# Kernel tuning notes

Measured on AMD Instinct MI355X. Metric: run time of the kernel, lower is better.

Reference implementation:

```python
import jax, jax.numpy as jnp
import numpy as np

B, S, D = 2, 1024, 2048
H, HK, HD = 16, 4, 128
E, TOPK, I = 16, 6, 1024
IS = 2048  # shared experts intermediate = moe_intermediate_size[0] * moe_num_shared_experts
EPS = 1e-6
NORM_MIN = 1e-12
SCALE = HD ** -0.5


def setup_inputs() -> dict:
    key = jax.random.key(0)
    ks = jax.random.split(key, 16)
    w = lambda k, *sh: jax.random.normal(k, sh, jnp.float32) * 0.02
    # interleaved RoPE tables (rotate_half_text pairs even/odd dims)
    inv_freq = 1.0 / (10000.0 ** (np.arange(0, HD, 2, dtype=np.float32) / HD))
    freqs = np.outer(np.arange(S, dtype=np.float32), inv_freq)        # [S, HD/2]
    emb = np.repeat(freqs, 2, axis=-1)                                 # [S, HD]
    cos = jnp.asarray(np.broadcast_to(np.cos(emb)[None], (B, S, HD)).copy())
    sin = jnp.asarray(np.broadcast_to(np.sin(emb)[None], (B, S, HD)).copy())
    return dict(
        hidden_states=jax.random.normal(ks[0], (B, S, D), jnp.float32),
        cos=cos, sin=sin,
        ln1_w=jnp.ones((D,), jnp.float32),
        ln2_w=jnp.ones((D,), jnp.float32),
        Wq=w(ks[1], D, H * HD), Wk=w(ks[2], D, HK * HD), Wv=w(ks[3], D, HK * HD), Wo=w(ks[4], H * HD, D),
        Wgate=w(ks[5], D, E),
        corr_bias=jnp.zeros((E,), jnp.float32),
        Wg=w(ks[6], E, D, I), Wu=w(ks[7], E, D, I), Wd=w(ks[8], E, I, D),
        Wgs=w(ks[9], D, IS), Wus=w(ks[10], D, IS), Wds=w(ks[11], IS, D),
    )


def rms_norm(x, weight, eps=EPS):
    xf = x.astype(jnp.float32)
    var = jnp.mean(xf * xf, axis=-1, keepdims=True)
    return (weight * (xf * jax.lax.rsqrt(var + eps))).astype(x.dtype)


def rotate_half(x):
    # interleaved variant: (x0, x1, x2, x3, ...) -> (-x1, x0, -x3, x2, ...)
    x1 = x[..., 0::2]
    x2 = x[..., 1::2]
    return jnp.stack((-x2, x1), axis=-1).reshape(x.shape)


def apply_rope(q, k, cos, sin):
    # q: [B,H,S,HD], k: [B,HK,S,HD], cos/sin: [B,S,HD] -> unsqueeze head dim
    c = cos[:, None].astype(jnp.float32)
    s = sin[:, None].astype(jnp.float32)
    qe = (q.astype(jnp.float32) * c + rotate_half(q).astype(jnp.float32) * s).astype(q.dtype)
    ke = (k.astype(jnp.float32) * c + rotate_half(k).astype(jnp.float32) * s).astype(k.dtype)
    return qe, ke


def attention(x, cos, sin, Wq, Wk, Wv, Wo):
    b, s, _ = x.shape
    q = (x @ Wq).reshape(b, s, H, HD).transpose(0, 2, 1, 3)    # [B,H,S,HD]
    k = (x @ Wk).reshape(b, s, HK, HD).transpose(0, 2, 1, 3)   # [B,HK,S,HD]
    v = (x @ Wv).reshape(b, s, HK, HD).transpose(0, 2, 1, 3)
    q, k = apply_rope(q, k, cos, sin)
    rep = H // HK
    k = jnp.repeat(k, rep, axis=1)
    v = jnp.repeat(v, rep, axis=1)
    scores = jnp.einsum('bhqd,bhkd->bhqk', q, k).astype(jnp.float32) * SCALE
    mask = jnp.triu(jnp.full((s, s), jnp.finfo(jnp.float32).min, jnp.float32), 1)
    attn = jax.nn.softmax(scores + mask, axis=-1).astype(x.dtype)
    out = jnp.einsum('bhqk,bhkd->bhqd', attn, v)
    out = out.transpose(0, 2, 1, 3).reshape(b, s, H * HD)
    return out @ Wo


def moe(x, Wgate, corr_bias, Wg, Wu, Wd, Wgs, Wus, Wds):
    b, s, d = x.shape
    # shared experts (dense SwiGLU MLP)
    shared = (jax.nn.silu(x @ Wgs) * (x @ Wus)) @ Wds
    xt = x.reshape(-1, d)                                       # [T, D]
    T = xt.shape[0]
    logits = xt.astype(jnp.float32) @ Wgate                     # float32 gate
    probs = jax.nn.softmax(logits, axis=-1)
    _, sel = jax.lax.top_k(probs + corr_bias, TOPK)             # [T, K]
    rw = jnp.take_along_axis(probs, sel, axis=-1)               # gather un-corrected probs
    rw = rw / jnp.clip(jnp.sum(rw, axis=-1, keepdims=True), NORM_MIN)
    # dense routing matrix [T, E] (zero for unselected experts == index_add semantics)
    route = jnp.zeros((T, E), jnp.float32).at[jnp.arange(T)[:, None], sel].set(rw)
    route = route.astype(x.dtype)
    # run all experts densely, mask with routing weights
    g = jnp.einsum('td,edi->tei', xt, Wg)
    u = jnp.einsum('td,edi->tei', xt, Wu)
    eo = jnp.einsum('tei,eid->ted', jax.nn.silu(g) * u, Wd)     # per-expert down proj
    y = jnp.einsum('ted,te->td', eo, route).reshape(b, s, d)
    return y + shared


def reference(hidden_states, cos, sin, ln1_w, ln2_w, Wq, Wk, Wv, Wo,
              Wgate, corr_bias, Wg, Wu, Wd, Wgs, Wus, Wds):
    residual = hidden_states
    h = rms_norm(hidden_states, ln1_w)
    h = attention(h, cos, sin, Wq, Wk, Wv, Wo)
    h = residual + h
    residual = h
    h = rms_norm(h, ln2_w)
    h = moe(h, Wgate, corr_bias, Wg, Wu, Wd, Wgs, Wus, Wds)
    return residual + h
```

## Files before the change

kernel.cpp:

```cpp
#include <hip/hip_runtime.h>
#include <cstdint>

typedef unsigned short u16;
typedef __attribute__((ext_vector_type(8))) short short8;
typedef __attribute__((ext_vector_type(4))) short s16x4;
typedef __attribute__((ext_vector_type(4))) float f32x4;

#define MFMA_16x16x32(a,b,c) __builtin_amdgcn_mfma_f32_16x16x32_bf16(a,b,c,0,0,0)

#define GLDS16(lds, g) __builtin_amdgcn_global_load_lds( \
    (const __attribute__((address_space(1))) unsigned int*)(g), \
    (__attribute__((address_space(3))) unsigned int*)(lds), 16, 0, 0)

#define BB 2
#define SS 1024
#define DD 2048
#define HH 16
#define HKK 4
#define HDD 128
#define EE 16
#define NTOP 6
#define II 1024
#define ISS 2048
#define TT 2048
#define CAP 2048

__device__ __forceinline__ u16 f2b(float f) {
    union { float f; uint32_t u; } v; v.f = f;
    uint32_t r = v.u + 0x7FFFu + ((v.u >> 16) & 1u);
    return (u16)(r >> 16);
}
__device__ __forceinline__ float b2f(u16 h) {
    union { uint32_t u; float f; } v; v.u = ((uint32_t)h) << 16;
    return v.f;
}
__device__ __forceinline__ void fsplit(float f, u16& hi, u16& lo) {
    u16 h = f2b(f);
    hi = h;
    lo = f2b(f - b2f(h));
}

template<bool SPLIT>
__global__ __launch_bounds__(256) void k_prep(
    const float* __restrict__ In, u16* __restrict__ Oh, u16* __restrict__ Ol,
    int R, int C)
{
    const size_t zoff = (size_t)blockIdx.z * R * C;
    In += zoff; Oh += zoff; if (SPLIT) Ol += zoff;
    const int r0 = blockIdx.y * 32, c0 = blockIdx.x * 32;
    __shared__ float tile[32][33];
    const int tx = threadIdx.x & 31, ty = threadIdx.x >> 5;
    #pragma unroll
    for (int i = 0; i < 4; ++i)
        tile[ty + i*8][tx] = In[(size_t)(r0 + ty + i*8)*C + c0 + tx];
    __syncthreads();
    const int c = threadIdx.x >> 3, rs = (threadIdx.x & 7) * 4;
    s16x4 hv, lv;
    #pragma unroll
    for (int j = 0; j < 4; ++j) {
        float f = tile[rs + j][c];
        u16 hb = f2b(f);
        hv[j] = (short)hb;
        if (SPLIT) lv[j] = (short)f2b(f - b2f(hb));
        else lv[j] = 0;
    }
    *(s16x4*)(Oh + (size_t)(c0 + c)*R + r0 + rs) = hv;
    if (SPLIT) *(s16x4*)(Ol + (size_t)(c0 + c)*R + r0 + rs) = lv;
}

__global__ __launch_bounds__(256) void k_rmsnorm_split(
    const float* __restrict__ X, const float* __restrict__ Wt,
    u16* __restrict__ Oh, u16* __restrict__ Ol)
{
    const int t = blockIdx.x;
    const float* x = X + (size_t)t * DD;
    const int base = threadIdx.x * 8;
    f32x4 v0 = *(const f32x4*)(x + base);
    f32x4 v1 = *(const f32x4*)(x + base + 4);
    float ss = 0.f;
    #pragma unroll
    for (int j = 0; j < 4; ++j) ss += v0[j]*v0[j] + v1[j]*v1[j];
    #pragma unroll
    for (int o = 1; o < 64; o <<= 1) ss += __shfl_xor(ss, o);
    __shared__ float red[4];
    if ((threadIdx.x & 63) == 0) red[threadIdx.x >> 6] = ss;
    __syncthreads();
    float tot = red[0] + red[1] + red[2] + red[3];
    float inv = rsqrtf(tot * (1.0f/DD) + 1e-6f);
    f32x4 w0 = *(const f32x4*)(Wt + base);
    f32x4 w1 = *(const f32x4*)(Wt + base + 4);
    u16* oh = Oh + (size_t)t*DD + base;
    u16* ol = Ol + (size_t)t*DD + base;
    #pragma unroll
    for (int j = 0; j < 4; ++j) {
        float y0 = v0[j]*inv*w0[j];
        float y1 = v1[j]*inv*w1[j];
        fsplit(y0, oh[j],   ol[j]);
        fsplit(y1, oh[4+j], ol[4+j]);
    }
}

__global__ __launch_bounds__(256) void k_rmsnorm_bf(
    const float* __restrict__ X, const float* __restrict__ Wt,
    u16* __restrict__ Ob, float* __restrict__ Of)
{
    const int t = blockIdx.x;
    const float* x = X + (size_t)t * DD;
    const int base = threadIdx.x * 8;
    f32x4 v0 = *(const f32x4*)(x + base);
    f32x4 v1 = *(const f32x4*)(x + base + 4);
    float ss = 0.f;
    #pragma unroll
    for (int j = 0; j < 4; ++j) ss += v0[j]*v0[j] + v1[j]*v1[j];
    #pragma unroll
    for (int o = 1; o < 64; o <<= 1) ss += __shfl_xor(ss, o);
    __shared__ float red[4];
    if ((threadIdx.x & 63) == 0) red[threadIdx.x >> 6] = ss;
    __syncthreads();
    float tot = red[0] + red[1] + red[2] + red[3];
    float inv = rsqrtf(tot * (1.0f/DD) + 1e-6f);
    f32x4 w0 = *(const f32x4*)(Wt + base);
    f32x4 w1 = *(const f32x4*)(Wt + base + 4);
    u16* ob = Ob + (size_t)t*DD + base;
    float* of = Of + (size_t)t*DD + base;
    #pragma unroll
    for (int j = 0; j < 4; ++j) {
        float y0 = v0[j]*inv*w0[j];
        float y1 = v1[j]*inv*w1[j];
        ob[j] = f2b(y0); ob[4+j] = f2b(y1);
        of[j] = y0;      of[4+j] = y1;
    }
}

template<int EPI>
__global__ __launch_bounds__(256) void k_gemm_hi(
    const u16* __restrict__ Ah, const u16* __restrict__ Al,
    const u16* __restrict__ Bth, const u16* __restrict__ Btl,
    float* __restrict__ C, const float* __restrict__ Res,
    int M, int N, int K)
{
    __shared__ u16 Ash[128][32];
    __shared__ u16 Asl[128][32];
    __shared__ u16 Bsh[128][32];
    __shared__ u16 Bsl[128][32];
    const int tid = threadIdx.x;
    const int lane = tid & 63;
    const int w = tid >> 6;
    const int m0 = blockIdx.y * 128, n0 = blockIdx.x * 128;
    const int wm = (w >> 1) * 64, wn = (w & 1) * 64;
    const int l15 = lane & 15, lhi = lane >> 4;
    f32x4 acc[4][4];
    #pragma unroll
    for (int a = 0; a < 4; ++a)
        #pragma unroll
        for (int b = 0; b < 4; ++b) acc[a][b] = 0;

    const int gr = w*32 + (lane >> 2);
    const int gc = (lane & 3) * 8;
    const u16* ahP0 = Ah  + (size_t)(m0 + gr) * K + gc;
    const u16* alP0 = Al  + (size_t)(m0 + gr) * K + gc;
    const u16* bhP0 = Bth + (size_t)(n0 + gr) * K + gc;
    const u16* blP0 = Btl + (size_t)(n0 + gr) * K + gc;
    const size_t r16 = (size_t)16 * K;

    for (int k0 = 0; k0 < K; k0 += 32) {
        __syncthreads();
        GLDS16(&Ash[w*32][0],      ahP0 + k0);
        GLDS16(&Ash[w*32 + 16][0], ahP0 + r16 + k0);
        GLDS16(&Asl[w*32][0],      alP0 + k0);
        GLDS16(&Asl[w*32 + 16][0], alP0 + r16 + k0);
        GLDS16(&Bsh[w*32][0],      bhP0 + k0);
        GLDS16(&Bsh[w*32 + 16][0], bhP0 + r16 + k0);
        GLDS16(&Bsl[w*32][0],      blP0 + k0);
        GLDS16(&Bsl[w*32 + 16][0], blP0 + r16 + k0);
        __syncthreads();
        short8 afh[4], afl[4], bfh[4], bfl[4];
        #pragma unroll
        for (int i = 0; i < 4; ++i) {
            afh[i] = *(const short8*)&Ash[wm + i*16 + l15][lhi*8];
            afl[i] = *(const short8*)&Asl[wm + i*16 + l15][lhi*8];
            bfh[i] = *(const short8*)&Bsh[wn + i*16 + l15][lhi*8];
            bfl[i] = *(const short8*)&Bsl[wn + i*16 + l15][lhi*8];
        }
        #pragma unroll
        for (int a = 0; a < 4; ++a)
            #pragma unroll
            for (int b = 0; b < 4; ++b) {
                acc[a][b] = MFMA_16x16x32(afh[a], bfh[b], acc[a][b]);
                acc[a][b] = MFMA_16x16x32(afh[a], bfl[b], acc[a][b]);
                acc[a][b] = MFMA_16x16x32(afl[a], bfh[b], acc[a][b]);
            }
    }
    #pragma unroll
    for (int a = 0; a < 4; ++a)
      #pragma unroll
      for (int b = 0; b < 4; ++b)
        #pragma unroll
        for (int r = 0; r < 4; ++r) {
            int m = m0 + wm + a*16 + lhi*4 + r;
            int n = n0 + wn + b*16 + l15;
            size_t off = (size_t)m * N + n;
            float v = acc[a][b][r];
            if (EPI == 1) C[off] = v + Res[off];
            else C[off] = v;
        }
}

template<int EPI>
__global__ __launch_bounds__(256) void k_gemm(
    const u16* __restrict__ A, const u16* __restrict__ Bt,
    void* __restrict__ C, int M, int N, int K)
{
    __shared__ u16 As[128][32];
    __shared__ u16 Bs[128][32];
    const int tid = threadIdx.x;
    const int lane = tid & 63;
    const int w = tid >> 6;
    const int m0 = blockIdx.y * 128, n0 = blockIdx.x * 128;
    const int wm = (w >> 1) * 64, wn = (w & 1) * 64;
    const int l15 = lane & 15, lhi = lane >> 4;
    f32x4 acc[4][4];
    #pragma unroll
    for (int a = 0; a < 4; ++a)
        #pragma unroll
        for (int b = 0; b < 4; ++b) acc[a][b] = 0;

    const int gr = w*32 + (lane >> 2);
    const int gc = (lane & 3) * 8;
    const u16* aP0 = A  + (size_t)(m0 + gr) * K + gc;
    const u16* bP0 = Bt + (size_t)(n0 + gr) * K + gc;
    const size_t r16 = (size_t)16 * K;

    for (int k0 = 0; k0 < K; k0 += 32) {
        __syncthreads();
        GLDS16(&As[w*32][0],      aP0 + k0);
        GLDS16(&As[w*32 + 16][0], aP0 + r16 + k0);
        GLDS16(&Bs[w*32][0],      bP0 + k0);
        GLDS16(&Bs[w*32 + 16][0], bP0 + r16 + k0);
        __syncthreads();
        short8 af[4], bf[4];
        #pragma unroll
        for (int i = 0; i < 4; ++i) af[i] = *(const short8*)&As[wm + i*16 + l15][lhi*8];
        #pragma unroll
        for (int i = 0; i < 4; ++i) bf[i] = *(const short8*)&Bs[wn + i*16 + l15][lhi*8];
        #pragma unroll
        for (int a = 0; a < 4; ++a)
            #pragma unroll
            for (int b = 0; b < 4; ++b)
                acc[a][b] = MFMA_16x16x32(af[a], bf[b], acc[a][b]);
    }
    #pragma unroll
    for (int a = 0; a < 4; ++a)
      #pragma unroll
      for (int b = 0; b < 4; ++b)
        #pragma unroll
        for (int r = 0; r < 4; ++r) {
            int m = m0 + wm + a*16 + lhi*4 + r;
            int n = n0 + wn + b*16 + l15;
            size_t off = (size_t)m * N + n;
            float v = acc[a][b][r];
            if (EPI == 0) ((u16*)C)[off] = f2b(v);
            else ((float*)C)[off] = v;
        }
}

template<bool GATHER>
__global__ __launch_bounds__(256) void k_glu(
    const u16* __restrict__ Xb, const u16* __restrict__ W1t,
    const u16* __restrict__ W2t, u16* __restrict__ Hout,
    const int* __restrict__ list, const int* __restrict__ cntp,
    int M, int NE, int K)
{
    const int e = GATHER ? blockIdx.z : 0;
    const int cnt = GATHER ? cntp[e] : M;
    const int m0 = blockIdx.y * 128;
    if (m0 >= cnt) return;
    const int n0 = blockIdx.x * 64;
    const u16* w1 = W1t + (size_t)e * NE * K;
    const u16* w2 = W2t + (size_t)e * NE * K;
    u16* hout = Hout + (size_t)e * CAP * NE;
    const int* lst = GATHER ? (list + e * CAP) : nullptr;

    __shared__ u16 As[128][32];
    __shared__ u16 B1s[64][32];
    __shared__ u16 B2s[64][32];

    const int tid = threadIdx.x, lane = tid & 63, w = tid >> 6;
    const int wm = (w >> 1) * 64, wn = (w & 1) * 32;
    const int l15 = lane & 15, lhi = lane >> 4;
    f32x4 acc1[4][2], acc2[4][2];
    #pragma unroll
    for (int a = 0; a < 4; ++a)
        #pragma unroll
        for (int j = 0; j < 2; ++j) { acc1[a][j] = 0; acc2[a][j] = 0; }

    const int gr  = w*32 + (lane >> 2);
    const int grB = w*16 + (lane >> 2);
    const int gc  = (lane & 3) * 8;
    int arow0, arow1;
    if (GATHER) {
        int mr0 = m0 + gr, mr1 = m0 + gr + 16;
        arow0 = (mr0 < cnt) ? (lst[mr0] >> 3) : 0;
        arow1 = (mr1 < cnt) ? (lst[mr1] >> 3) : 0;
    } else { arow0 = m0 + gr; arow1 = m0 + gr + 16; }
    const u16* aP0 = Xb + (size_t)arow0 * K + gc;
    const u16* aP1 = Xb + (size_t)arow1 * K + gc;
    const u16* b1P = w1 + (size_t)(n0 + grB) * K + gc;
    const u16* b2P = w2 + (size_t)(n0 + grB) * K + gc;

    for (int k0 = 0; k0 < K; k0 += 32) {
        __syncthreads();
        GLDS16(&As[w*32][0],      aP0 + k0);
        GLDS16(&As[w*32 + 16][0], aP1 + k0);
        GLDS16(&B1s[w*16][0],     b1P + k0);
        GLDS16(&B2s[w*16][0],     b2P + k0);
        __syncthreads();
        short8 af[4], b1[2], b2[2];
        #pragma unroll
        for (int i = 0; i < 4; ++i) af[i] = *(const short8*)&As[wm + i*16 + l15][lhi*8];
        #pragma unroll
        for (int j = 0; j < 2; ++j) {
            b1[j] = *(const short8*)&B1s[wn + j*16 + l15][lhi*8];
            b2[j] = *(const short8*)&B2s[wn + j*16 + l15][lhi*8];
        }
        #pragma unroll
        for (int a = 0; a < 4; ++a)
            #pragma unroll
            for (int j = 0; j < 2; ++j) {
                acc1[a][j] = MFMA_16x16x32(af[a], b1[j], acc1[a][j]);
                acc2[a][j] = MFMA_16x16x32(af[a], b2[j], acc2[a][j]);
            }
    }
    #pragma unroll
    for (int a = 0; a < 4; ++a)
      #pragma unroll
      for (int j = 0; j < 2; ++j)
        #pragma unroll
        for (int r = 0; r < 4; ++r) {
            int m = m0 + wm + a*16 + lhi*4 + r;
            if (m < cnt) {
                int n = n0 + wn + j*16 + l15;
                float g = acc1[a][j][r], u = acc2[a][j][r];
                float hval = g / (1.0f + __expf(-g)) * u;
                hout[(size_t)m * NE + n] = f2b(hval);
            }
        }
}

__global__ __launch_bounds__(256) void k_down_scatter(
    const u16* __restrict__ Hb, const u16* __restrict__ WdTt,
    u16* __restrict__ Rbuf, const int* __restrict__ list,
    const float* __restrict__ wts, const int* __restrict__ cntp,
    int N, int K)
{
    const int e = blockIdx.z;
    const int cnt = cntp[e];
    const int m0 = blockIdx.y * 128;
    if (m0 >= cnt) return;
    const int n0 = blockIdx.x * 128;
    const u16* A  = Hb   + (size_t)e * CAP * K;
    const u16* Bt = WdTt + (size_t)e * N * K;

    __shared__ u16 As[128][32];
    __shared__ u16 Bs[128][32];
    const int tid = threadIdx.x, lane = tid & 63, w = tid >> 6;
    const int wm = (w >> 1) * 64, wn = (w & 1) * 64;
    const int l15 = lane & 15, lhi = lane >> 4;
    f32x4 acc[4][4];
    #pragma unroll
    for (int a = 0; a < 4; ++a)
        #pragma unroll
        for (int b = 0; b < 4; ++b) acc[a][b] = 0;

    const int gr = w*32 + (lane >> 2);
    const int gc = (lane & 3) * 8;
    const u16* aP0 = A  + (size_t)(m0 + gr) * K + gc;
    const u16* bP0 = Bt + (size_t)(n0 + gr) * K + gc;
    const size_t r16 = (size_t)16 * K;

    for (int k0 = 0; k0 < K; k0 += 32) {
        __syncthreads();
        GLDS16(&As[w*32][0],      aP0 + k0);
        GLDS16(&As[w*32 + 16][0], aP0 + r16 + k0);
        GLDS16(&Bs[w*32][0],      bP0 + k0);
        GLDS16(&Bs[w*32 + 16][0], bP0 + r16 + k0);
        __syncthreads();
        short8 af[4], bf[4];
        #pragma unroll
        for (int i = 0; i < 4; ++i) af[i] = *(const short8*)&As[wm + i*16 + l15][lhi*8];
        #pragma unroll
        for (int i = 0; i < 4; ++i) bf[i] = *(const short8*)&Bs[wn + i*16 + l15][lhi*8];
        #pragma unroll
        for (int a = 0; a < 4; ++a)
            #pragma unroll
            for (int b = 0; b < 4; ++b)
                acc[a][b] = MFMA_16x16x32(af[a], bf[b], acc[a][b]);
    }
    #pragma unroll
    for (int a = 0; a < 4; ++a)
      #pragma unroll
      for (int b = 0; b < 4; ++b)
        #pragma unroll
        for (int r = 0; r < 4; ++r) {
            int m = m0 + wm + a*16 + lhi*4 + r;
            if (m < cnt) {
                int n = n0 + wn + b*16 + l15;
                int enc = list[e*CAP + m];
                float wgt = wts[e*CAP + m];
                int tok = enc >> 3, kk = enc & 7;
                Rbuf[((size_t)tok*NTOP + kk)*N + n] = f2b(acc[a][b][r] * wgt);
            }
        }
}

__global__ __launch_bounds__(256) void k_rope_f32(
    float* __restrict__ QKV,
    const float* __restrict__ Cs, const float* __restrict__ Sn)
{
    int id = blockIdx.x * 256 + threadIdx.x;
    int pr = id & 63;
    int rest = id >> 6;
    int hh = rest % 20;
    int tok = rest / 20;
    if (tok >= TT) return;
    int d0 = pr * 2;
    float c0 = Cs[(size_t)tok*HDD + d0];
    float c1 = Cs[(size_t)tok*HDD + d0 + 1];
    float s0 = Sn[(size_t)tok*HDD + d0];
    float s1 = Sn[(size_t)tok*HDD + d0 + 1];
    float* p = QKV + (size_t)tok*3072 + (hh < HH ? hh*HDD : 2048 + (hh - HH)*HDD);
    float x0 = p[d0], x1 = p[d0+1];
    p[d0]     = x0*c0 - x1*s0;
    p[d0 + 1] = x1*c1 + x0*s1;
}

__global__ __launch_bounds__(256) void k_split_s(
    const float* __restrict__ X, int stride, int cols,
    u16* __restrict__ Hi, u16* __restrict__ Lo)
{
    int id = blockIdx.x * 256 + threadIdx.x;
    int base = id * 8;
    int t = base / cols;
    int c = base - t * cols;
    const float* in = X + (size_t)t * stride + c;
    f32x4 v0 = *(const f32x4*)in;
    f32x4 v1 = *(const f32x4*)(in + 4);
    u16* h = Hi + (size_t)t * cols + c;
    u16* l = Lo + (size_t)t * cols + c;
    #pragma unroll
    for (int j = 0; j < 4; ++j) {
        fsplit(v0[j], h[j],   l[j]);
        fsplit(v1[j], h[4+j], l[4+j]);
    }
}

__global__ __launch_bounds__(256) void k_split_vt(
    const float* __restrict__ QKV, u16* __restrict__ Vth, u16* __restrict__ Vtl)
{
    int id = blockIdx.x * 256 + threadIdx.x;
    int oid = id * 8;
    int s0 = oid & (SS - 1);
    int r = oid >> 10;
    int d = r & (HDD - 1);
    int bh = r >> 7;
    int b = bh >> 2, hk = bh & 3;
    #pragma unroll
    for (int j = 0; j < 8; ++j) {
        int s = s0 + j;
        float v = QKV[(size_t)(b*SS + s)*3072 + 2560 + hk*HDD + d];
        fsplit(v, Vth[oid + j], Vtl[oid + j]);
    }
}

__global__ __launch_bounds__(256) void k_attn_hi(
    const u16* __restrict__ Qh, const u16* __restrict__ Ql,
    const u16* __restrict__ Kh, const u16* __restrict__ Kl,
    const u16* __restrict__ Vth, const u16* __restrict__ Vtl,
    u16* __restrict__ Oh, u16* __restrict__ Ol)
{
    const int tid = threadIdx.x;
    const int lane = tid & 63;
    const int w = tid >> 6;
    const int q0 = blockIdx.x * 64;
    const int b = blockIdx.y >> 4;
    const int h = blockIdx.y & 15;
    const int hk = h >> 2;
    const int l15 = lane & 15, lhi = lane >> 4;

    __shared__ u16 Ksh[32][136];
    __shared__ u16 Ksl[32][136];
    __shared__ u16 Vsh[128][40];
    __shared__ u16 Vsl[128][40];
    __shared__ u16 Psh[4][16][40];
    __shared__ u16 Psl[4][16][40];

    short8 qfh[4], qfl[4];
    {
        const int qrow = q0 + w*16 + l15;
        const u16* qph = Qh + ((size_t)(b*SS + qrow)*HH + h)*HDD;
        const u16* qpl = Ql + ((size_t)(b*SS + qrow)*HH + h)*HDD;
        #pragma unroll
        for (int c = 0; c < 4; ++c) {
            qfh[c] = *(const short8*)(qph + c*32 + lhi*8);
            qfl[c] = *(const short8*)(qpl + c*32 + lhi*8);
        }
    }

    f32x4 oacc[8];
    #pragma unroll
    for (int ch = 0; ch < 8; ++ch) oacc[ch] = 0;
    float m_r[4] = {-1e30f, -1e30f, -1e30f, -1e30f};
    float l_r[4] = {0.f, 0.f, 0.f, 0.f};

    const int nkt = (q0 + 64) >> 5;
    const int kr = tid >> 3, kc = (tid & 7) * 16;
    const int vd = tid >> 1, vj = (tid & 1) * 16;

    for (int kt = 0; kt < nkt; ++kt) {
        __syncthreads();
        {
            size_t koff = ((size_t)(b*SS + kt*32 + kr)*HKK + hk)*HDD + kc;
            *(short8*)&Ksh[kr][kc]     = *(const short8*)(Kh + koff);
            *(short8*)&Ksh[kr][kc + 8] = *(const short8*)(Kh + koff + 8);
            *(short8*)&Ksl[kr][kc]     = *(const short8*)(Kl + koff);
            *(short8*)&Ksl[kr][kc + 8] = *(const short8*)(Kl + koff + 8);
        }
        {
            size_t voff = ((size_t)(b*HKK + hk)*HDD + vd)*SS + kt*32 + vj;
            *(short8*)&Vsh[vd][vj]     = *(const short8*)(Vth + voff);
            *(short8*)&Vsh[vd][vj + 8] = *(const short8*)(Vth + voff + 8);
            *(short8*)&Vsl[vd][vj]     = *(const short8*)(Vtl + voff);
            *(short8*)&Vsl[vd][vj + 8] = *(const short8*)(Vtl + voff + 8);
        }
        __syncthreads();

        f32x4 s0 = 0, s1 = 0;
        #pragma unroll
        for (int c = 0; c < 4; ++c) {
            short8 kh0 = *(const short8*)&Ksh[l15][c*32 + lhi*8];
            short8 kl0 = *(const short8*)&Ksl[l15][c*32 + lhi*8];
            short8 kh1 = *(const short8*)&Ksh[16 + l15][c*32 + lhi*8];
            short8 kl1 = *(const short8*)&Ksl[16 + l15][c*32 + lhi*8];
            s0 = MFMA_16x16x32(qfh[c], kh0, s0);
            s0 = MFMA_16x16x32(qfh[c], kl0, s0);
            s0 = MFMA_16x16x32(qfl[c], kh0, s0);
            s1 = MFMA_16x16x32(qfh[c], kh1, s1);
            s1 = MFMA_16x16x32(qfh[c], kl1, s1);
            s1 = MFMA_16x16x32(qfl[c], kh1, s1);
        }
        const int irow0 = q0 + w*16 + lhi*4;
        const int j0 = kt*32 + l15;
        float ef[4];
        #pragma unroll
        for (int r = 0; r < 4; ++r) {
            float a0 = s0[r] * 0.08838834764831845f;
            float a1 = s1[r] * 0.08838834764831845f;
            const int ir = irow0 + r;
            if (j0 > ir) a0 = -1e30f;
            if (j0 + 16 > ir) a1 = -1e30f;
            float mx = fmaxf(a0, a1);
            #pragma unroll
            for (int o = 1; o < 16; o <<= 1) mx = fmaxf(mx, __shfl_xor(mx, o));
            float mn = fmaxf(m_r[r], mx);
            ef[r] = __expf(m_r[r] - mn);
            m_r[r] = mn;
            float p0 = __expf(a0 - mn);
            float p1 = __expf(a1 - mn);
            float ps = p0 + p1;
            #pragma unroll
            for (int o = 1; o < 16; o <<= 1) ps += __shfl_xor(ps, o);
            l_r[r] = l_r[r]*ef[r] + ps;
            fsplit(p0, Psh[w][lhi*4 + r][l15],      Psl[w][lhi*4 + r][l15]);
            fsplit(p1, Psh[w][lhi*4 + r][16 + l15], Psl[w][lhi*4 + r][16 + l15]);
        }
        #pragma unroll
        for (int ch = 0; ch < 8; ++ch) {
            f32x4 t = oacc[ch];
            t[0] *= ef[0]; t[1] *= ef[1]; t[2] *= ef[2]; t[3] *= ef[3];
            oacc[ch] = t;
        }
        __syncthreads();
        short8 pah = *(const short8*)&Psh[w][l15][lhi*8];
        short8 pal = *(const short8*)&Psl[w][l15][lhi*8];
        #pragma unroll
        for (int ch = 0; ch < 8; ++ch) {
            short8 bvh = *(const short8*)&Vsh[ch*16 + l15][lhi*8];
            short8 bvl = *(const short8*)&Vsl[ch*16 + l15][lhi*8];
            oacc[ch] = MFMA_16x16x32(pah, bvh, oacc[ch]);
            oacc[ch] = MFMA_16x16x32(pah, bvl, oacc[ch]);
            oacc[ch] = MFMA_16x16x32(pal, bvh, oacc[ch]);
        }
    }
    #pragma unroll
    for (int r = 0; r < 4; ++r) {
        const int row = q0 + w*16 + lhi*4 + r;
        const float inv = 1.0f / l_r[r];
        u16* oph = Oh + ((size_t)(b*SS + row)*HH + h)*HDD;
        u16* opl = Ol + ((size_t)(b*SS + row)*HH + h)*HDD;
        #pragma unroll
        for (int ch = 0; ch < 8; ++ch) {
            float o = oacc[ch][r] * inv;
            fsplit(o, oph[ch*16 + l15], opl[ch*16 + l15]);
        }
    }
}

__global__ __launch_bounds__(256) void k_router(
    const float* __restrict__ X, const float* __restrict__ Wg,
    const float* __restrict__ bias,
    int* __restrict__ cnt, int* __restrict__ list, float* __restrict__ wts)
{
    const int t = blockIdx.x;
    const int e = threadIdx.x & 15, sl = threadIdx.x >> 4;
    const float* x = X + (size_t)t * DD;
    float part = 0.f;
    for (int i = 0; i < 128; ++i) {
        int k = sl * 128 + i;
        part += x[k] * Wg[(size_t)k * EE + e];
    }
    __shared__ float red[16][17];
    red[sl][e] = part;
    __syncthreads();
    if (threadIdx.x == 0) {
        float lg[16], pr[16];
        for (int ee = 0; ee < 16; ++ee) {
            float s = 0.f;
            for (int q = 0; q < 16; ++q) s += red[q][ee];
            lg[ee] = s;
        }
        float mx = lg[0];
        for (int ee = 1; ee < 16; ++ee) mx = fmaxf(mx, lg[ee]);
        float sum = 0.f;
        for (int ee = 0; ee < 16; ++ee) { pr[ee] = expf(lg[ee] - mx); sum += pr[ee]; }
        float isum = 1.0f / sum;
        for (int ee = 0; ee < 16; ++ee) pr[ee] *= isum;
        unsigned used = 0;
        int sel[NTOP]; float rw[NTOP]; float s6 = 0.f;
        for (int kk = 0; kk < NTOP; ++kk) {
            int best = 0; float bv = -1e30f;
            for (int ee = 0; ee < 16; ++ee) {
                if (used & (1u << ee)) continue;
                float sc = pr[ee] + bias[ee];
                if (sc > bv) { bv = sc; best = ee; }
            }
            used |= 1u << best;
            sel[kk] = best; rw[kk] = pr[best]; s6 += pr[best];
        }
        float inv6 = 1.0f / fmaxf(s6, 1e-12f);
        for (int kk = 0; kk < NTOP; ++kk) {
            int ee = sel[kk];
            int pos = atomicAdd(&cnt[ee], 1);
            list[ee*CAP + pos] = (t << 3) | kk;
            wts[ee*CAP + pos] = rw[kk] * inv6;
        }
    }
}

__global__ __launch_bounds__(256) void k_final(
    const float* __restrict__ h2, const float* __restrict__ yb,
    const u16* __restrict__ rb, float* __restrict__ out)
{
    int id = blockIdx.x * 256 + threadIdx.x;
    size_t i4 = (size_t)id * 4;
    int t = id >> 9;
    int d = (id & 511) * 4;
    f32x4 acc = *(const f32x4*)(h2 + i4);
    f32x4 y = *(const f32x4*)(yb + i4);
    acc += y;
    #pragma unroll
    for (int kk = 0; kk < NTOP; ++kk) {
        s16x4 rv = *(const s16x4*)(rb + ((size_t)t*NTOP + kk)*DD + d);
        acc[0] += b2f((u16)rv[0]); acc[1] += b2f((u16)rv[1]);
        acc[2] += b2f((u16)rv[2]); acc[3] += b2f((u16)rv[3]);
    }
    *(f32x4*)(out + i4) = acc;
}

extern "C" void kernel_launch(void* const* d_in, const int* in_sizes, int n_in,
                              void* d_out, int out_size, void* d_ws, size_t ws_size,
                              hipStream_t stream)
{
    (void)in_sizes; (void)n_in; (void)out_size; (void)ws_size;
    const float* hidden = (const float*)d_in[0];
    const float* cosb   = (const float*)d_in[1];
    const float* sinb   = (const float*)d_in[2];
    const float* ln1    = (const float*)d_in[3];
    const float* ln2    = (const float*)d_in[4];
    const float* Wq     = (const float*)d_in[5];
    const float* Wk     = (const float*)d_in[6];
    const float* Wv     = (const float*)d_in[7];
    const float* Wo     = (const float*)d_in[8];
    const float* Wgate  = (const float*)d_in[9];
    const float* cbias  = (const float*)d_in[10];
    const float* Wg     = (const float*)d_in[11];
    const float* Wu     = (const float*)d_in[12];
    const float* Wd     = (const float*)d_in[13];
    const float* Wgs    = (const float*)d_in[14];
    const float* Wus    = (const float*)d_in[15];
    const float* Wds    = (const float*)d_in[16];
    float* out = (float*)d_out;

    char* ws = (char*)d_ws;
    size_t off = 0;
    auto alloc = [&](size_t bytes) {
        void* p = ws + off;
        off = (off + bytes + 255) & ~(size_t)255;
        return p;
    };
    u16* WqkvTh = (u16*)alloc((size_t)3072*2048*2);
    u16* WqkvTl = (u16*)alloc((size_t)3072*2048*2);
    u16* WoTh   = (u16*)alloc((size_t)2048*2048*2);
    u16* WoTl   = (u16*)alloc((size_t)2048*2048*2);
    u16* WgsT   = (u16*)alloc((size_t)2048*2048*2);
    u16* WusT   = (u16*)alloc((size_t)2048*2048*2);
    u16* WdsT   = (u16*)alloc((size_t)2048*2048*2);
    u16* WgT    = (u16*)alloc((size_t)EE*II*DD*2);
    u16* WuT    = (u16*)alloc((size_t)EE*II*DD*2);
    u16* WdT    = (u16*)alloc((size_t)EE*DD*II*2);
    u16*   x1h  = (u16*)  alloc((size_t)TT*DD*2);
    u16*   x1l  = (u16*)  alloc((size_t)TT*DD*2);
    float* qkvf = (float*)alloc((size_t)TT*3072*4);
    u16*   qh   = (u16*)  alloc((size_t)TT*HH*HDD*2);
    u16*   ql   = (u16*)  alloc((size_t)TT*HH*HDD*2);
    u16*   kh   = (u16*)  alloc((size_t)TT*HKK*HDD*2);
    u16*   kl   = (u16*)  alloc((size_t)TT*HKK*HDD*2);
    u16*   vth  = (u16*)  alloc((size_t)TT*HKK*HDD*2);
    u16*   vtl  = (u16*)  alloc((size_t)TT*HKK*HDD*2);
    u16*   aoh  = (u16*)  alloc((size_t)TT*HH*HDD*2);
    u16*   aol  = (u16*)  alloc((size_t)TT*HH*HDD*2);
    float* h2   = (float*)alloc((size_t)TT*DD*4);
    u16*   x2   = (u16*)  alloc((size_t)TT*DD*2);
    float* x2f  = (float*)alloc((size_t)TT*DD*4);
    int*   cnt  = (int*)  alloc(256);
    int*   lst  = (int*)  alloc((size_t)EE*CAP*4);
    float* wts  = (float*)alloc((size_t)EE*CAP*4);
    u16*   hE   = (u16*)  alloc((size_t)EE*CAP*II*2);
    u16*   rbuf = (u16*)  alloc((size_t)TT*NTOP*DD*2);
    u16*   hs   = x1h;
    float* ybuf = qkvf;

    k_prep<true ><<<dim3(64,64,1), 256, 0, stream>>>(Wq, WqkvTh, WqkvTl, 2048, 2048);
    k_prep<true ><<<dim3(16,64,1), 256, 0, stream>>>(Wk, WqkvTh + (size_t)2048*2048, WqkvTl + (size_t)2048*2048, 2048, 512);
    k_prep<true ><<<dim3(16,64,1), 256, 0, stream>>>(Wv, WqkvTh + (size_t)2560*2048, WqkvTl + (size_t)2560*2048, 2048, 512);
    k_prep<true ><<<dim3(64,64,1), 256, 0, stream>>>(Wo, WoTh, WoTl, 2048, 2048);
    k_prep<false><<<dim3(64,64,1), 256, 0, stream>>>(Wgs, WgsT, nullptr, 2048, 2048);
    k_prep<false><<<dim3(64,64,1), 256, 0, stream>>>(Wus, WusT, nullptr, 2048, 2048);
    k_prep<false><<<dim3(64,64,1), 256, 0, stream>>>(Wds, WdsT, nullptr, 2048, 2048);
    k_prep<false><<<dim3(32,64,EE), 256, 0, stream>>>(Wg, WgT, nullptr, 2048, 1024);
    k_prep<false><<<dim3(32,64,EE), 256, 0, stream>>>(Wu, WuT, nullptr, 2048, 1024);
    k_prep<false><<<dim3(64,32,EE), 256, 0, stream>>>(Wd, WdT, nullptr, 1024, 2048);

    k_rmsnorm_split<<<TT, 256, 0, stream>>>(hidden, ln1, x1h, x1l);
    k_gemm_hi<2><<<dim3(24,16), 256, 0, stream>>>(x1h, x1l, WqkvTh, WqkvTl, qkvf, nullptr, TT, 3072, DD);
    k_rope_f32<<<(TT*20*64)/256, 256, 0, stream>>>(qkvf, cosb, sinb);
    k_split_s<<<(TT*2048/8)/256, 256, 0, stream>>>(qkvf, 3072, 2048, qh, ql);
    k_split_s<<<(TT*512/8)/256, 256, 0, stream>>>(qkvf + 2048, 3072, 512, kh, kl);
    k_split_vt<<<(TT*HKK*HDD/8)/256, 256, 0, stream>>>(qkvf, vth, vtl);
    k_attn_hi<<<dim3(SS/64, BB*HH), 256, 0, stream>>>(qh, ql, kh, kl, vth, vtl, aoh, aol);
    k_gemm_hi<1><<<dim3(16,16), 256, 0, stream>>>(aoh, aol, WoTh, WoTl, h2, hidden, TT, DD, HH*HDD);

    k_rmsnorm_bf<<<TT, 256, 0, stream>>>(h2, ln2, x2, x2f);
    hipMemsetAsync(cnt, 0, 256, stream);
    k_router<<<TT, 256, 0, stream>>>(x2f, Wgate, cbias, cnt, lst, wts);
    k_glu<false><<<dim3(ISS/64, TT/128, 1), 256, 0, stream>>>(x2, WgsT, WusT, hs, nullptr, nullptr, TT, ISS, DD);
    k_gemm<2><<<dim3(16,16), 256, 0, stream>>>(hs, WdsT, ybuf, TT, DD, ISS);
    k_glu<true><<<dim3(II/64, CAP/128, EE), 256, 0, stream>>>(x2, WgT, WuT, hE, lst, cnt, CAP, II, DD);
    k_down_scatter<<<dim3(DD/128, CAP/128, EE), 256, 0, stream>>>(hE, WdT, rbuf, lst, wts, cnt, DD, II);
    k_final<<<(TT*DD/4)/256, 256, 0, stream>>>(h2, ybuf, rbuf, out);
}
```

Measured before the change: 1.123 ms.

## Double-buffer LDS tiles in all GEMM kernels and fuse RoPE with bf16 split

Every MFMA GEMM kernel (hi/lo, plain, GLU, down-scatter) now keeps two LDS buffers. It prefetches the next K-slice with global_load_lds while computing on the current one, which cuts each iteration from two barriers to one. Separately, the RoPE kernel now writes split hi/lo bf16 Q and K directly, replacing the in-place fp32 update and two split kernels. The cost is doubled LDS per block, which may reduce occupancy. Overlap also depends on whether the async LDS loads are waited on only at the barrier.

```diff
diff --git a/kernel.cpp b/kernel.cpp
--- a/kernel.cpp
+++ b/kernel.cpp
@@ -139,10 +139,10 @@
     float* __restrict__ C, const float* __restrict__ Res,
     int M, int N, int K)
 {
-    __shared__ u16 Ash[128][32];
-    __shared__ u16 Asl[128][32];
-    __shared__ u16 Bsh[128][32];
-    __shared__ u16 Bsl[128][32];
+    __shared__ u16 Ash[2][128][32];
+    __shared__ u16 Asl[2][128][32];
+    __shared__ u16 Bsh[2][128][32];
+    __shared__ u16 Bsl[2][128][32];
     const int tid = threadIdx.x;
     const int lane = tid & 63;
     const int w = tid >> 6;
@@ -163,24 +163,36 @@
     const u16* blP0 = Btl + (size_t)(n0 + gr) * K + gc;
     const size_t r16 = (size_t)16 * K;
 
+    GLDS16(&Ash[0][w*32][0],      ahP0);
+    GLDS16(&Ash[0][w*32 + 16][0], ahP0 + r16);
+    GLDS16(&Asl[0][w*32][0],      alP0);
+    GLDS16(&Asl[0][w*32 + 16][0], alP0 + r16);
+    GLDS16(&Bsh[0][w*32][0],      bhP0);
+    GLDS16(&Bsh[0][w*32 + 16][0], bhP0 + r16);
+    GLDS16(&Bsl[0][w*32][0],      blP0);
+    GLDS16(&Bsl[0][w*32 + 16][0], blP0 + r16);
+    __syncthreads();
+
+    int cur = 0;
     for (int k0 = 0; k0 < K; k0 += 32) {
-        __syncthreads();
-        GLDS16(&Ash[w*32][0],      ahP0 + k0);
-        GLDS16(&Ash[w*32 + 16][0], ahP0 + r16 + k0);
-        GLDS16(&Asl[w*32][0],      alP0 + k0);
-        GLDS16(&Asl[w*32 + 16][0], alP0 + r16 + k0);
-        GLDS16(&Bsh[w*32][0],      bhP0 + k0);
-        GLDS16(&Bsh[w*32 + 16][0], bhP0 + r16 + k0);
-        GLDS16(&Bsl[w*32][0],      blP0 + k0);
-        GLDS16(&Bsl[w*32 + 16][0], blP0 + r16 + k0);
-        __syncthreads();
+        const int nxt = k0 + 32;
+        if (nxt < K) {
+            GLDS16(&Ash[cur^1][w*32][0],      ahP0 + nxt);
+            GLDS16(&Ash[cur^1][w*32 + 16][0], ahP0 + r16 + nxt);
+            GLDS16(&Asl[cur^1][w*32][0],      alP0 + nxt);
+            GLDS16(&Asl[cur^1][w*32 + 16][0], alP0 + r16 + nxt);
+            GLDS16(&Bsh[cur^1][w*32][0],      bhP0 + nxt);
+            GLDS16(&Bsh[cur^1][w*32 + 16][0], bhP0 + r16 + nxt);
+            GLDS16(&Bsl[cur^1][w*32][0],      blP0 + nxt);
+            GLDS16(&Bsl[cur^1][w*32 + 16][0], blP0 + r16 + nxt);
+        }
         short8 afh[4], afl[4], bfh[4], bfl[4];
         #pragma unroll
         for (int i = 0; i < 4; ++i) {
-            afh[i] = *(const short8*)&Ash[wm + i*16 + l15][lhi*8];
-            afl[i] = *(const short8*)&Asl[wm + i*16 + l15][lhi*8];
-            bfh[i] = *(const short8*)&Bsh[wn + i*16 + l15][lhi*8];
-            bfl[i] = *(const short8*)&Bsl[wn + i*16 + l15][lhi*8];
+            afh[i] = *(const short8*)&Ash[cur][wm + i*16 + l15][lhi*8];
+            afl[i] = *(const short8*)&Asl[cur][wm + i*16 + l15][lhi*8];
+            bfh[i] = *(const short8*)&Bsh[cur][wn + i*16 + l15][lhi*8];
+            bfl[i] = *(const short8*)&Bsl[cur][wn + i*16 + l15][lhi*8];
         }
         #pragma unroll
         for (int a = 0; a < 4; ++a)
@@ -190,6 +202,8 @@
                 acc[a][b] = MFMA_16x16x32(afh[a], bfl[b], acc[a][b]);
                 acc[a][b] = MFMA_16x16x32(afl[a], bfh[b], acc[a][b]);
             }
+        __syncthreads();
+        cur ^= 1;
     }
     #pragma unroll
     for (int a = 0; a < 4; ++a)
@@ -211,8 +225,8 @@
     const u16* __restrict__ A, const u16* __restrict__ Bt,
     void* __restrict__ C, int M, int N, int K)
 {
-    __shared__ u16 As[128][32];
-    __shared__ u16 Bs[128][32];
+    __shared__ u16 As[2][128][32];
+    __shared__ u16 Bs[2][128][32];
     const int tid = threadIdx.x;
     const int lane = tid & 63;
     const int w = tid >> 6;
@@ -231,23 +245,33 @@
     const u16* bP0 = Bt + (size_t)(n0 + gr) * K + gc;
     const size_t r16 = (size_t)16 * K;
 
+    GLDS16(&As[0][w*32][0],      aP0);
+    GLDS16(&As[0][w*32 + 16][0], aP0 + r16);
+    GLDS16(&Bs[0][w*32][0],      bP0);
+    GLDS16(&Bs[0][w*32 + 16][0], bP0 + r16);
+    __syncthreads();
+
+    int cur = 0;
     for (int k0 = 0; k0 < K; k0 += 32) {
-        __syncthreads();
-        GLDS16(&As[w*32][0],      aP0 + k0);
-        GLDS16(&As[w*32 + 16][0], aP0 + r16 + k0);
-        GLDS16(&Bs[w*32][0],      bP0 + k0);
-        GLDS16(&Bs[w*32 + 16][0], bP0 + r16 + k0);
-        __syncthreads();
+        const int nxt = k0 + 32;
+        if (nxt < K) {
+            GLDS16(&As[cur^1][w*32][0],      aP0 + nxt);
+            GLDS16(&As[cur^1][w*32 + 16][0], aP0 + r16 + nxt);
+            GLDS16(&Bs[cur^1][w*32][0],      bP0 + nxt);
+            GLDS16(&Bs[cur^1][w*32 + 16][0], bP0 + r16 + nxt);
+        }
         short8 af[4], bf[4];
         #pragma unroll
-        for (int i = 0; i < 4; ++i) af[i] = *(const short8*)&As[wm + i*16 + l15][lhi*8];
-        #pragma unroll
-        for (int i = 0; i < 4; ++i) bf[i] = *(const short8*)&Bs[wn + i*16 + l15][lhi*8];
+        for (int i = 0; i < 4; ++i) af[i] = *(const short8*)&As[cur][wm + i*16 + l15][lhi*8];
+        #pragma unroll
+        for (int i = 0; i < 4; ++i) bf[i] = *(const short8*)&Bs[cur][wn + i*16 + l15][lhi*8];
         #pragma unroll
         for (int a = 0; a < 4; ++a)
             #pragma unroll
             for (int b = 0; b < 4; ++b)
                 acc[a][b] = MFMA_16x16x32(af[a], bf[b], acc[a][b]);
+        __syncthreads();
+        cur ^= 1;
     }
     #pragma unroll
     for (int a = 0; a < 4; ++a)
@@ -281,9 +305,9 @@
     u16* hout = Hout + (size_t)e * CAP * NE;
     const int* lst = GATHER ? (list + e * CAP) : nullptr;
 
-    __shared__ u16 As[128][32];
-    __shared__ u16 B1s[64][32];
-    __shared__ u16 B2s[64][32];
+    __shared__ u16 As[2][128][32];
+    __shared__ u16 B1s[2][64][32];
+    __shared__ u16 B2s[2][64][32];
 
     const int tid = threadIdx.x, lane = tid & 63, w = tid >> 6;
     const int wm = (w >> 1) * 64, wn = (w & 1) * 32;
@@ -308,20 +332,28 @@
     const u16* b1P = w1 + (size_t)(n0 + grB) * K + gc;
     const u16* b2P = w2 + (size_t)(n0 + grB) * K + gc;
 
+    GLDS16(&As[0][w*32][0],      aP0);
+    GLDS16(&As[0][w*32 + 16][0], aP1);
+    GLDS16(&B1s[0][w*16][0],     b1P);
+    GLDS16(&B2s[0][w*16][0],     b2P);
+    __syncthreads();
+
+    int cur = 0;
     for (int k0 = 0; k0 < K; k0 += 32) {
-        __syncthreads();
-        GLDS16(&As[w*32][0],      aP0 + k0);
-        GLDS16(&As[w*32 + 16][0], aP1 + k0);
-        GLDS16(&B1s[w*16][0],     b1P + k0);
-        GLDS16(&B2s[w*16][0],     b2P + k0);
-        __syncthreads();
+        const int nxt = k0 + 32;
+        if (nxt < K) {
+            GLDS16(&As[cur^1][w*32][0],      aP0 + nxt);
+            GLDS16(&As[cur^1][w*32 + 16][0], aP1 + nxt);
+            GLDS16(&B1s[cur^1][w*16][0],     b1P + nxt);
+            GLDS16(&B2s[cur^1][w*16][0],     b2P + nxt);
+        }
         short8 af[4], b1[2], b2[2];
         #pragma unroll
-        for (int i = 0; i < 4; ++i) af[i] = *(const short8*)&As[wm + i*16 + l15][lhi*8];
+        for (int i = 0; i < 4; ++i) af[i] = *(const short8*)&As[cur][wm + i*16 + l15][lhi*8];
         #pragma unroll
         for (int j = 0; j < 2; ++j) {
-            b1[j] = *(const short8*)&B1s[wn + j*16 + l15][lhi*8];
-            b2[j] = *(const short8*)&B2s[wn + j*16 + l15][lhi*8];
+            b1[j] = *(const short8*)&B1s[cur][wn + j*16 + l15][lhi*8];
+            b2[j] = *(const short8*)&B2s[cur][wn + j*16 + l15][lhi*8];
         }
         #pragma unroll
         for (int a = 0; a < 4; ++a)
@@ -330,6 +362,8 @@
                 acc1[a][j] = MFMA_16x16x32(af[a], b1[j], acc1[a][j]);
                 acc2[a][j] = MFMA_16x16x32(af[a], b2[j], acc2[a][j]);
             }
+        __syncthreads();
+        cur ^= 1;
     }
     #pragma unroll
     for (int a = 0; a < 4; ++a)
@@ -361,8 +395,8 @@
     const u16* A  = Hb   + (size_t)e * CAP * K;
     const u16* Bt = WdTt + (size_t)e * N * K;
 
-    __shared__ u16 As[128][32];
-    __shared__ u16 Bs[128][32];
+    __shared__ u16 As[2][128][32];
+    __shared__ u16 Bs[2][128][32];
     const int tid = threadIdx.x, lane = tid & 63, w = tid >> 6;
     const int wm = (w >> 1) * 64, wn = (w & 1) * 64;
     const int l15 = lane & 15, lhi = lane >> 4;
@@ -378,23 +412,33 @@
     const u16* bP0 = Bt + (size_t)(n0 + gr) * K + gc;
     const size_t r16 = (size_t)16 * K;
 
+    GLDS16(&As[0][w*32][0],      aP0);
+    GLDS16(&As[0][w*32 + 16][0], aP0 + r16);
+    GLDS16(&Bs[0][w*32][0],      bP0);
+    GLDS16(&Bs[0][w*32 + 16][0], bP0 + r16);
+    __syncthreads();
+
+    int cur = 0;
     for (int k0 = 0; k0 < K; k0 += 32) {
-        __syncthreads();
-        GLDS16(&As[w*32][0],      aP0 + k0);
-        GLDS16(&As[w*32 + 16][0], aP0 + r16 + k0);
-        GLDS16(&Bs[w*32][0],      bP0 + k0);
-        GLDS16(&Bs[w*32 + 16][0], bP0 + r16 + k0);
-        __syncthreads();
+        const int nxt = k0 + 32;
+        if (nxt < K) {
+            GLDS16(&As[cur^1][w*32][0],      aP0 + nxt);
+            GLDS16(&As[cur^1][w*32 + 16][0], aP0 + r16 + nxt);
+            GLDS16(&Bs[cur^1][w*32][0],      bP0 + nxt);
+            GLDS16(&Bs[cur^1][w*32 + 16][0], bP0 + r16 + nxt);
+        }
         short8 af[4], bf[4];
         #pragma unroll
-        for (int i = 0; i < 4; ++i) af[i] = *(const short8*)&As[wm + i*16 + l15][lhi*8];
-        #pragma unroll
-        for (int i = 0; i < 4; ++i) bf[i] = *(const short8*)&Bs[wn + i*16 + l15][lhi*8];
+        for (int i = 0; i < 4; ++i) af[i] = *(const short8*)&As[cur][wm + i*16 + l15][lhi*8];
+        #pragma unroll
+        for (int i = 0; i < 4; ++i) bf[i] = *(const short8*)&Bs[cur][wn + i*16 + l15][lhi*8];
         #pragma unroll
         for (int a = 0; a < 4; ++a)
             #pragma unroll
             for (int b = 0; b < 4; ++b)
                 acc[a][b] = MFMA_16x16x32(af[a], bf[b], acc[a][b]);
+        __syncthreads();
+        cur ^= 1;
     }
     #pragma unroll
     for (int a = 0; a < 4; ++a)
@@ -413,9 +457,11 @@
         }
 }
 
-__global__ __launch_bounds__(256) void k_rope_f32(
-    float* __restrict__ QKV,
-    const float* __restrict__ Cs, const float* __restrict__ Sn)
+__global__ __launch_bounds__(256) void k_rope_split(
+    const float* __restrict__ QKV,
+    const float* __restrict__ Cs, const float* __restrict__ Sn,
+    u16* __restrict__ Qh, u16* __restrict__ Ql,
+    u16* __restrict__ Kh, u16* __restrict__ Kl)
 {
     int id = blockIdx.x * 256 + threadIdx.x;
     int pr = id & 63;
@@ -428,30 +474,16 @@
     float c1 = Cs[(size_t)tok*HDD + d0 + 1];
     float s0 = Sn[(size_t)tok*HDD + d0];
     float s1 = Sn[(size_t)tok*HDD + d0 + 1];
-    float* p = QKV + (size_t)tok*3072 + (hh < HH ? hh*HDD : 2048 + (hh - HH)*HDD);
+    const float* p = QKV + (size_t)tok*3072 + (hh < HH ? hh*HDD : 2048 + (hh - HH)*HDD);
     float x0 = p[d0], x1 = p[d0+1];
-    p[d0]     = x0*c0 - x1*s0;
-    p[d0 + 1] = x1*c1 + x0*s1;
-}
-
-__global__ __launch_bounds__(256) void k_split_s(
-    const float* __restrict__ X, int stride, int cols,
-    u16* __restrict__ Hi, u16* __restrict__ Lo)
-{
-    int id = blockIdx.x * 256 + threadIdx.x;
-    int base = id * 8;
-    int t = base / cols;
-    int c = base - t * cols;
-    const float* in = X + (size_t)t * stride + c;
-    f32x4 v0 = *(const f32x4*)in;
-    f32x4 v1 = *(const f32x4*)(in + 4);
-    u16* h = Hi + (size_t)t * cols + c;
-    u16* l = Lo + (size_t)t * cols + c;
-    #pragma unroll
-    for (int j = 0; j < 4; ++j) {
-        fsplit(v0[j], h[j],   l[j]);
-        fsplit(v1[j], h[4+j], l[4+j]);
-    }
+    float y0 = x0*c0 - x1*s0;
+    float y1 = x1*c1 + x0*s1;
+    u16 *oh, *ol;
+    size_t ooff;
+    if (hh < HH) { ooff = ((size_t)tok*HH + hh)*HDD + d0; oh = Qh; ol = Ql; }
+    else         { ooff = ((size_t)tok*HKK + (hh - HH))*HDD + d0; oh = Kh; ol = Kl; }
+    fsplit(y0, oh[ooff],     ol[ooff]);
+    fsplit(y1, oh[ooff + 1], ol[ooff + 1]);
 }
 
 __global__ __launch_bounds__(256) void k_split_vt(
@@ -752,15 +784,13 @@
 
     k_rmsnorm_split<<<TT, 256, 0, stream>>>(hidden, ln1, x1h, x1l);
     k_gemm_hi<2><<<dim3(24,16), 256, 0, stream>>>(x1h, x1l, WqkvTh, WqkvTl, qkvf, nullptr, TT, 3072, DD);
-    k_rope_f32<<<(TT*20*64)/256, 256, 0, stream>>>(qkvf, cosb, sinb);
-    k_split_s<<<(TT*2048/8)/256, 256, 0, stream>>>(qkvf, 3072, 2048, qh, ql);
-    k_split_s<<<(TT*512/8)/256, 256, 0, stream>>>(qkvf + 2048, 3072, 512, kh, kl);
+    k_rope_split<<<(TT*20*64)/256, 256, 0, stream>>>(qkvf, cosb, sinb, qh, ql, kh, kl);
     k_split_vt<<<(TT*HKK*HDD/8)/256, 256, 0, stream>>>(qkvf, vth, vtl);
     k_attn_hi<<<dim3(SS/64, BB*HH), 256, 0, stream>>>(qh, ql, kh, kl, vth, vtl, aoh, aol);
     k_gemm_hi<1><<<dim3(16,16), 256, 0, stream>>>(aoh, aol, WoTh, WoTl, h2, hidden, TT, DD, HH*HDD);
 
     k_rmsnorm_bf<<<TT, 256, 0, stream>>>(h2, ln2, x2, x2f);
-    hipMemsetAsync(cnt, 0, 256, stream);
+    (void)hipMemsetAsync(cnt, 0, 256, stream);
     k_router<<<TT, 256, 0, stream>>>(x2f, Wgate, cbias, cnt, lst, wts);
     k_glu<false><<<dim3(ISS/64, TT/128, 1), 256, 0, stream>>>(x2, WgsT, WusT, hs, nullptr, nullptr, TT, ISS, DD);
     k_gemm<2><<<dim3(16,16), 256, 0, stream>>>(hs, WdsT, ybuf, TT, DD, ISS);
```

Result: faster. 1.093 ms (-2.7%).
